# Kernel tuning notes

Hardware: AMD Instinct MI355X
Metric: run time of the kernel (lower is better)

Reference implementation:

```python
import jax, jax.numpy as jnp
import numpy as np

S = 20  # number of standard amino acids; hardcoded in the original layer


def expm_fixed(A, squarings=6, terms=14):
    """Scaling-and-squaring matrix exponential with fixed squaring count.
    A: (..., n, n). tau*Q entries are small (tau ~ softplus(-3)), so a fixed
    2^-6 scaling + Taylor-14 matches tf.linalg.expm to fp32 tolerance."""
    A = A / (2.0 ** squarings)
    I = jnp.broadcast_to(jnp.eye(A.shape[-1], dtype=A.dtype), A.shape)
    out = I
    term = I
    for i in range(1, terms + 1):
        term = jnp.matmul(term, A) / i
        out = out + term
    for _ in range(squarings):
        out = jnp.matmul(out, out)
    return out


def make_rate_matrix(R, p, eps=1e-16):
    """R: (N, s, s) symmetric exchangeabilities, zero diag. p: (N, s) equilibrium."""
    Q = R * p[:, None, :]                       # Q[i,j] = R[i,j] * p[j]
    diag = jnp.sum(Q, axis=-1, keepdims=True)   # (N, s, 1)
    eye = jnp.eye(Q.shape[-1], dtype=Q.dtype)
    Q = Q - diag * eye
    mue = jnp.sum(p[:, :, None] * diag, axis=-2, keepdims=True)  # (N,1,1)
    return Q / jnp.maximum(mue, eps)


def setup_inputs() -> dict:
    key = jax.random.key(0)
    ks = jax.random.split(key, 6)
    m, b, L, k, nr = 2, 256, 1024, 4, 100
    inputs = jax.random.uniform(ks[0], (m, b, L, S), dtype=jnp.float32)
    rate_indices = jax.random.randint(ks[1], (m, b), 0, nr, dtype=jnp.int64)
    # rate_init = constant(-3.0); small jitter so gradients are non-degenerate
    tau_kernel = -3.0 + 0.1 * jax.random.normal(ks[2], (m, nr), dtype=jnp.float32)
    exchangeability_kernel = 0.1 * jax.random.normal(ks[3], (m, k, S, S), dtype=jnp.float32)
    equilibrium_kernel = 0.1 * jax.random.normal(ks[4], (m, k, S), dtype=jnp.float32)
    per_matrix_rates_kernel = 0.1 * jax.random.normal(ks[5], (m, k), dtype=jnp.float32)
    return {
        "inputs": inputs,
        "tau_kernel": tau_kernel,
        "exchangeability_kernel": exchangeability_kernel,
        "equilibrium_kernel": equilibrium_kernel,
        "per_matrix_rates_kernel": per_matrix_rates_kernel,
        "rate_indices": rate_indices,
    }


def reference(inputs, tau_kernel, exchangeability_kernel, equilibrium_kernel,
              per_matrix_rates_kernel, rate_indices):
    m, b, L, s = inputs.shape
    k = exchangeability_kernel.shape[1]
    # make_tau(subset): gather per-sequence times then softplus
    tau = jax.nn.softplus(jnp.take_along_axis(tau_kernel, rate_indices, axis=1))  # (m,b)
    # per-matrix rates
    pmr = jax.nn.softplus(per_matrix_rates_kernel)  # (m,k)
    mut_rates = tau[:, :, None] * pmr[:, None, :]   # (m,b,k)
    # make_R: symmetrize, softplus, zero diagonal
    K = exchangeability_kernel
    R = jax.nn.softplus(0.5 * (K + jnp.swapaxes(K, -1, -2)))
    R = R * (1.0 - jnp.eye(s, dtype=R.dtype))       # (m,k,s,s)
    # make_p
    p = jax.nn.softmax(equilibrium_kernel, axis=-1)  # (m,k,s)
    # normalized rate matrices
    Q = make_rate_matrix(R.reshape(-1, s, s), p.reshape(-1, s)).reshape(m, k, s, s)
    # tau * Q, batched over sequences: (m,b,k,s,s)
    tauQ = mut_rates[..., None, None] * Q[:, None]
    P = expm_fixed(tauQ.reshape(-1, s, s)).reshape(m, b, k, s, s)
    # vector-format inputs path (non-transposed): mbLz,mbkzs->mbLks
    anc = jnp.einsum('mblz,mbkzs->mblks', inputs, P)
    # documented output: (num_model, b, L, num_matrices*s)
    return anc.reshape(m, b, L, k * s)
```

## Files before the change

kernel.cpp:

```cpp
#include <hip/hip_runtime.h>
#include <math.h>

#define M_  2
#define B_  256
#define L_  1024
#define K_  4
#define S_  20
#define NR_ 100

__device__ __forceinline__ float softplusf(float x) {
    return x > 20.0f ? x : log1pf(expf(x));
}

__global__ __launch_bounds__(512)
void expm_kernel(const float* __restrict__ tauk,
                 const float* __restrict__ exch,
                 const float* __restrict__ equil,
                 const float* __restrict__ pmrk,
                 float*       __restrict__ Pws)
{
    __shared__ float sA[400];
    __shared__ float sT[2][400];
    __shared__ float sRow[20];

    const int blk = blockIdx.x;
    const int kk = blk % K_;
    const int rr = (blk / K_) % NR_;
    const int mm = blk / (K_ * NR_);

    const int tid = threadIdx.x;
    const bool act = tid < 400;
    const int i = tid / 20;
    const int j = tid - i * 20;

    float p[20];
    float Q0 = 0.0f, rowsum = 0.0f;

    if (act) {
        const float* eq = equil + (mm * K_ + kk) * S_;
        float mx = eq[0];
        #pragma unroll
        for (int z = 1; z < 20; ++z) mx = fmaxf(mx, eq[z]);
        float s = 0.0f;
        #pragma unroll
        for (int z = 0; z < 20; ++z) { p[z] = expf(eq[z] - mx); s += p[z]; }
        const float inv = 1.0f / s;
        #pragma unroll
        for (int z = 0; z < 20; ++z) p[z] *= inv;

        const float* Kx = exch + (mm * K_ + kk) * S_ * S_;
        float R = (i == j) ? 0.0f : softplusf(0.5f * (Kx[i * 20 + j] + Kx[j * 20 + i]));
        Q0 = R * p[j];
        sA[tid] = Q0;
    }
    __syncthreads();

    if (act) {
        rowsum = 0.0f;
        #pragma unroll
        for (int z = 0; z < 20; ++z) rowsum += sA[i * 20 + z];
        if (j == 0) sRow[i] = rowsum;
    }
    __syncthreads();

    float o = 0.0f;
    if (act) {
        float mue = 0.0f;
        #pragma unroll
        for (int z = 0; z < 20; ++z) mue += p[z] * sRow[z];
        float q = (Q0 - ((i == j) ? rowsum : 0.0f)) / fmaxf(mue, 1e-16f);

        const float tau = softplusf(tauk[mm * NR_ + rr]);
        const float pm  = softplusf(pmrk[mm * K_ + kk]);
        const float a = q * tau * pm;
        sA[tid] = a;
        sT[0][tid] = a;
        o = ((i == j) ? 1.0f : 0.0f) + a;
    }
    __syncthreads();

    int cur = 0;
    for (int it = 2; it <= 12; ++it) {
        if (act) {
            float acc = 0.0f;
            #pragma unroll
            for (int z = 0; z < 20; ++z) acc += sT[cur][i * 20 + z] * sA[z * 20 + j];
            acc /= (float)it;
            o += acc;
            sT[cur ^ 1][tid] = acc;
        }
        __syncthreads();
        cur ^= 1;
    }

    if (act) Pws[(size_t)blk * 400 + tid] = o;
}

#define RPB 128
#define TPB 320

__device__ __forceinline__ void fma4(float4& a, float s, const float4& p) {
    a.x = fmaf(s, p.x, a.x);
    a.y = fmaf(s, p.y, a.y);
    a.z = fmaf(s, p.z, a.z);
    a.w = fmaf(s, p.w, a.w);
}

__global__ __launch_bounds__(TPB)
void einsum_kernel(const float* __restrict__ inp,
                   const float* __restrict__ Pws,
                   const int*   __restrict__ ridx,
                   float*       __restrict__ out)
{
    __shared__ float Pl[K_ * 400];
    __shared__ float inL[RPB * 20];

    const int bx    = blockIdx.x;
    const int chunk = bx & 7;
    const int mb    = bx >> 3;
    const int mm    = mb >> 8;
    const int tid   = threadIdx.x;

    const int r = ridx[mb];

    {
        const float4* Psrc = (const float4*)(Pws + ((size_t)(mm * NR_ + r) * K_) * 400);
        float4* Pd = (float4*)Pl;
        for (int idx = tid; idx < 400; idx += TPB) Pd[idx] = Psrc[idx];

        const float4* Isrc = (const float4*)(inp + ((size_t)mb * L_ + chunk * RPB) * 20);
        float4* Id = (float4*)inL;
        for (int idx = tid; idx < RPB * 5; idx += TPB) Id[idx] = Isrc[idx];
    }
    __syncthreads();

    const int t  = tid % 20;
    const int rg = tid / 20;
    const int k  = t / 5;
    const int s0 = (t - k * 5) * 4;
    const float* Pk = Pl + k * 400 + s0;

    float4 acc[8];
    #pragma unroll
    for (int r8 = 0; r8 < 8; ++r8) acc[r8] = make_float4(0.f, 0.f, 0.f, 0.f);

    #pragma unroll
    for (int z4 = 0; z4 < 5; ++z4) {
        const float4 p0 = *(const float4*)(Pk + (z4 * 4 + 0) * 20);
        const float4 p1 = *(const float4*)(Pk + (z4 * 4 + 1) * 20);
        const float4 p2 = *(const float4*)(Pk + (z4 * 4 + 2) * 20);
        const float4 p3 = *(const float4*)(Pk + (z4 * 4 + 3) * 20);
        #pragma unroll
        for (int r8 = 0; r8 < 8; ++r8) {
            const int l = rg + r8 * 16;
            const float4 av = *(const float4*)(inL + l * 20 + z4 * 4);
            fma4(acc[r8], av.x, p0);
            fma4(acc[r8], av.y, p1);
            fma4(acc[r8], av.z, p2);
            fma4(acc[r8], av.w, p3);
        }
    }

    float* ob = out + ((size_t)mb * L_ + chunk * RPB) * 80;
    #pragma unroll
    for (int r8 = 0; r8 < 8; ++r8) {
        const int l = rg + r8 * 16;
        *(float4*)(ob + l * 80 + t * 4) = acc[r8];
    }
}

extern "C" void kernel_launch(void* const* d_in, const int* in_sizes, int n_in,
                              void* d_out, int out_size, void* d_ws, size_t ws_size,
                              hipStream_t stream) {
    const float* inp   = (const float*)d_in[0];
    const float* tauk  = (const float*)d_in[1];
    const float* exch  = (const float*)d_in[2];
    const float* equil = (const float*)d_in[3];
    const float* pmrk  = (const float*)d_in[4];
    const int*   ridx  = (const int*)d_in[5];
    float* outp = (float*)d_out;
    float* Pws  = (float*)d_ws;

    expm_kernel<<<M_ * NR_ * K_, 512, 0, stream>>>(tauk, exch, equil, pmrk, Pws);
    einsum_kernel<<<M_ * B_ * (L_ / RPB), TPB, 0, stream>>>(inp, Pws, ridx, outp);
}
```

Baseline: 60.59 us.

## Precompute scaled powers of Q per matrix and form P in the einsum kernel

Instead of computing a Taylor expm for every (model, rate, matrix) triple, the first kernel now computes Q^n/n! for n=1..7 only once per (model, matrix), which is 8 blocks instead of 800. The einsum kernel then builds P = I + sum mu^n Q^n/n! on the fly from the per-sequence time scale. This removes most of the expm launch work and relies on tau*Q being small enough for a 7-term series. The cost is that every einsum block now reads 7x more workspace data and does a small polynomial evaluation, and truncating at 7 terms (down from 12) risks accuracy loss.

```diff
diff --git a/kernel.cpp b/kernel.cpp
--- a/kernel.cpp
+++ b/kernel.cpp
@@ -7,27 +7,24 @@
 #define K_  4
 #define S_  20
 #define NR_ 100
+#define NTERM 7
 
 __device__ __forceinline__ float softplusf(float x) {
     return x > 20.0f ? x : log1pf(expf(x));
 }
 
 __global__ __launch_bounds__(512)
-void expm_kernel(const float* __restrict__ tauk,
-                 const float* __restrict__ exch,
+void qpow_kernel(const float* __restrict__ exch,
                  const float* __restrict__ equil,
-                 const float* __restrict__ pmrk,
-                 float*       __restrict__ Pws)
+                 float*       __restrict__ Qpow)
 {
-    __shared__ float sA[400];
+    __shared__ float sQ[400];
     __shared__ float sT[2][400];
     __shared__ float sRow[20];
 
     const int blk = blockIdx.x;
     const int kk = blk % K_;
-    const int rr = (blk / K_) % NR_;
-    const int mm = blk / (K_ * NR_);
-
+    const int mm = blk / K_;
     const int tid = threadIdx.x;
     const bool act = tid < 400;
     const int i = tid / 20;
@@ -51,49 +48,43 @@
         const float* Kx = exch + (mm * K_ + kk) * S_ * S_;
         float R = (i == j) ? 0.0f : softplusf(0.5f * (Kx[i * 20 + j] + Kx[j * 20 + i]));
         Q0 = R * p[j];
-        sA[tid] = Q0;
+        sQ[tid] = Q0;
     }
     __syncthreads();
 
     if (act) {
         rowsum = 0.0f;
         #pragma unroll
-        for (int z = 0; z < 20; ++z) rowsum += sA[i * 20 + z];
+        for (int z = 0; z < 20; ++z) rowsum += sQ[i * 20 + z];
         if (j == 0) sRow[i] = rowsum;
     }
     __syncthreads();
 
-    float o = 0.0f;
+    float* Tout = Qpow + (size_t)blk * (NTERM * 400);
     if (act) {
         float mue = 0.0f;
         #pragma unroll
         for (int z = 0; z < 20; ++z) mue += p[z] * sRow[z];
         float q = (Q0 - ((i == j) ? rowsum : 0.0f)) / fmaxf(mue, 1e-16f);
-
-        const float tau = softplusf(tauk[mm * NR_ + rr]);
-        const float pm  = softplusf(pmrk[mm * K_ + kk]);
-        const float a = q * tau * pm;
-        sA[tid] = a;
-        sT[0][tid] = a;
-        o = ((i == j) ? 1.0f : 0.0f) + a;
+        sQ[tid] = q;
+        sT[0][tid] = q;
+        Tout[tid] = q;
     }
     __syncthreads();
 
     int cur = 0;
-    for (int it = 2; it <= 12; ++it) {
+    for (int n = 2; n <= NTERM; ++n) {
         if (act) {
             float acc = 0.0f;
             #pragma unroll
-            for (int z = 0; z < 20; ++z) acc += sT[cur][i * 20 + z] * sA[z * 20 + j];
-            acc /= (float)it;
-            o += acc;
+            for (int z = 0; z < 20; ++z) acc += sT[cur][i * 20 + z] * sQ[z * 20 + j];
+            acc /= (float)n;
             sT[cur ^ 1][tid] = acc;
+            Tout[(n - 1) * 400 + tid] = acc;
         }
         __syncthreads();
         cur ^= 1;
     }
-
-    if (act) Pws[(size_t)blk * 400 + tid] = o;
 }
 
 #define RPB 128
@@ -108,12 +99,15 @@
 
 __global__ __launch_bounds__(TPB)
 void einsum_kernel(const float* __restrict__ inp,
-                   const float* __restrict__ Pws,
+                   const float* __restrict__ Qpow,
+                   const float* __restrict__ tauk,
+                   const float* __restrict__ pmrk,
                    const int*   __restrict__ ridx,
                    float*       __restrict__ out)
 {
     __shared__ float Pl[K_ * 400];
     __shared__ float inL[RPB * 20];
+    __shared__ float sMu[K_];
 
     const int bx    = blockIdx.x;
     const int chunk = bx & 7;
@@ -123,14 +117,29 @@
 
     const int r = ridx[mb];
 
+    if (tid < K_) {
+        const float tau = softplusf(tauk[mm * NR_ + r]);
+        const float pm  = softplusf(pmrk[mm * K_ + tid]);
+        sMu[tid] = tau * pm;
+    }
+
     {
-        const float4* Psrc = (const float4*)(Pws + ((size_t)(mm * NR_ + r) * K_) * 400);
-        float4* Pd = (float4*)Pl;
-        for (int idx = tid; idx < 400; idx += TPB) Pd[idx] = Psrc[idx];
-
         const float4* Isrc = (const float4*)(inp + ((size_t)mb * L_ + chunk * RPB) * 20);
         float4* Id = (float4*)inL;
         for (int idx = tid; idx < RPB * 5; idx += TPB) Id[idx] = Isrc[idx];
+    }
+    __syncthreads();
+
+    for (int idx = tid; idx < K_ * 400; idx += TPB) {
+        const int kk = idx / 400;
+        const int el = idx - kk * 400;
+        const float* T = Qpow + ((size_t)(mm * K_ + kk) * NTERM) * 400 + el;
+        const float mu = sMu[kk];
+        float acc = (el % 21 == 0) ? 1.0f : 0.0f;
+        float mp = mu;
+        #pragma unroll
+        for (int n = 0; n < NTERM; ++n) { acc = fmaf(mp, T[n * 400], acc); mp *= mu; }
+        Pl[idx] = acc;
     }
     __syncthreads();
 
@@ -179,8 +188,8 @@
     const float* pmrk  = (const float*)d_in[4];
     const int*   ridx  = (const int*)d_in[5];
     float* outp = (float*)d_out;
-    float* Pws  = (float*)d_ws;
+    float* Qpow = (float*)d_ws;
 
-    expm_kernel<<<M_ * NR_ * K_, 512, 0, stream>>>(tauk, exch, equil, pmrk, Pws);
-    einsum_kernel<<<M_ * B_ * (L_ / RPB), TPB, 0, stream>>>(inp, Pws, ridx, outp);
+    qpow_kernel<<<M_ * K_, 512, 0, stream>>>(exch, equil, Qpow);
+    einsum_kernel<<<M_ * B_ * (L_ / RPB), TPB, 0, stream>>>(inp, Qpow, tauk, pmrk, ridx, outp);
 }
```

After: 62.77 us. +3.6%, slower.
